# Kernel tuning notes

Measured on AMD Instinct MI355X. Metric: run time of the kernel, lower is better.

The kernel has to match this reference:

```python
import jax, jax.numpy as jnp
import numpy as np

N = 50000      # nodes
E = 800000     # edges (before self loops)
D_IN = 128
HID = 64
HEADS = 8
D_OUT = 10


def setup_inputs() -> dict:
    key = jax.random.key(0)
    ks = jax.random.split(key, 16)
    sc = 0.05
    x = jax.random.normal(ks[0], (N, D_IN), dtype=jnp.float32)
    edge_index = jax.random.randint(ks[1], (2, E), 0, N, dtype=jnp.int64)
    return {
        "x": x,
        "edge_index": edge_index,
        "W1": jax.random.normal(ks[2], (HEADS * HID, D_IN), dtype=jnp.float32) * sc,
        "a1_src": jax.random.normal(ks[3], (HEADS, HID), dtype=jnp.float32) * sc,
        "a1_dst": jax.random.normal(ks[4], (HEADS, HID), dtype=jnp.float32) * sc,
        "b1": jnp.zeros((HEADS * HID,), jnp.float32),
        "W2": jax.random.normal(ks[5], (HID, HEADS * HID), dtype=jnp.float32) * sc,
        "a2_src": jax.random.normal(ks[6], (1, HID), dtype=jnp.float32) * sc,
        "a2_dst": jax.random.normal(ks[7], (1, HID), dtype=jnp.float32) * sc,
        "b2": jnp.zeros((HID,), jnp.float32),
        "W3": jax.random.normal(ks[8], (HID, HID), dtype=jnp.float32) * sc,
        "a3_src": jax.random.normal(ks[9], (1, HID), dtype=jnp.float32) * sc,
        "a3_dst": jax.random.normal(ks[10], (1, HID), dtype=jnp.float32) * sc,
        "b3": jnp.zeros((HID,), jnp.float32),
        "Wc": jax.random.normal(ks[11], (D_OUT, HID), dtype=jnp.float32) * sc,
        "bc": jnp.zeros((D_OUT,), jnp.float32),
    }


def gat_conv(x, src, dst, W, a_src, a_dst, b, concat):
    """PyG GATConv (eval mode, add_self_loops already applied to src/dst)."""
    heads, out_ch = a_src.shape
    n = x.shape[0]
    h = (x @ W.T).reshape(n, heads, out_ch)          # [N, H, C]
    a_s = jnp.einsum('nhc,hc->nh', h, a_src)          # [N, H]
    a_d = jnp.einsum('nhc,hc->nh', h, a_dst)          # [N, H]
    e = jax.nn.leaky_relu(a_s[src] + a_d[dst], 0.2)   # [Etot, H]
    # segment softmax over incoming edges of each destination node
    m = jax.ops.segment_max(e, dst, num_segments=n)
    ex = jnp.exp(e - m[dst])
    s = jax.ops.segment_sum(ex, dst, num_segments=n)
    alpha = ex / (s[dst] + 1e-16)                     # [Etot, H]
    out = jax.ops.segment_sum(h[src] * alpha[:, :, None], dst, num_segments=n)
    if concat:
        out = out.reshape(n, heads * out_ch)
    else:
        out = out.mean(axis=1)
    return out + b


def reference(x, edge_index, W1, a1_src, a1_dst, b1, W2, a2_src, a2_dst, b2,
              W3, a3_src, a3_dst, b3, Wc, bc):
    loops = jnp.arange(N, dtype=edge_index.dtype)
    src = jnp.concatenate([edge_index[0], loops])
    dst = jnp.concatenate([edge_index[1], loops])
    h = jax.nn.elu(gat_conv(x, src, dst, W1, a1_src, a1_dst, b1, True))
    h = jax.nn.elu(gat_conv(h, src, dst, W2, a2_src, a2_dst, b2, False))
    h = jax.nn.elu(gat_conv(h, src, dst, W3, a3_src, a3_dst, b3, False))
    return h @ Wc.T + bc
```

## Files before the change

kernel.cpp:

```cpp
#include <hip/hip_runtime.h>
#include <math.h>

#define N_NODES 50000
#define N_EDGES 800000
#define ETOT    (N_EDGES + N_NODES)
#define COL_CAP (ETOT + 3 * N_NODES + 64)

typedef short bf16x8 __attribute__((ext_vector_type(8)));
typedef float f32x4  __attribute__((ext_vector_type(4)));
typedef float f32x2  __attribute__((ext_vector_type(2)));

__device__ __forceinline__ float b2f(unsigned int u16) {
    return __uint_as_float(u16 << 16);
}
__device__ __forceinline__ unsigned short f2b(float f) {
    unsigned int u = __float_as_uint(f);
    u += 0x7fffu + ((u >> 16) & 1u);
    return (unsigned short)(u >> 16);
}

__global__ __launch_bounds__(256) void k_prep(const float* __restrict__ x,
                                              const float* __restrict__ w1,
                                              const float* __restrict__ w2,
                                              const float* __restrict__ w3,
                                              const float* __restrict__ a1s,
                                              const float* __restrict__ a1d,
                                              unsigned short* __restrict__ xb,
                                              unsigned short* __restrict__ o1,
                                              unsigned short* __restrict__ o2,
                                              unsigned short* __restrict__ o3,
                                              float* __restrict__ U,
                                              int* __restrict__ deg,
                                              int* __restrict__ flag) {
    int i = blockIdx.x * 256 + threadIdx.x;
    if (i < N_NODES) deg[i] = 0;
    if (i == 0) *flag = 0;
    if (blockIdx.x < 8) {
        int h = blockIdx.x;
        int which = threadIdx.x >> 7, k = threadIdx.x & 127;
        const float* av = which ? a1d : a1s;
        float acc = 0.f;
        for (int c = 0; c < 64; ++c)
            acc += av[h * 64 + c] * w1[(size_t)(h * 64 + c) * 128 + k];
        U[(which * 8 + h) * 128 + k] = acc;
    }
    if (i < 512 * 128 / 4) {
        float4 v = ((const float4*)w1)[i];
        ushort2* o = (ushort2*)(o1 + i * 4);
        o[0] = make_ushort2(f2b(v.x), f2b(v.y));
        o[1] = make_ushort2(f2b(v.z), f2b(v.w));
    }
    if (i < 64 * 512 / 4) {
        float4 v = ((const float4*)w2)[i];
        ushort2* o = (ushort2*)(o2 + i * 4);
        o[0] = make_ushort2(f2b(v.x), f2b(v.y));
        o[1] = make_ushort2(f2b(v.z), f2b(v.w));
    }
    if (i < 64 * 64 / 4) {
        float4 v = ((const float4*)w3)[i];
        ushort2* o = (ushort2*)(o3 + i * 4);
        o[0] = make_ushort2(f2b(v.x), f2b(v.y));
        o[1] = make_ushort2(f2b(v.z), f2b(v.w));
    }
    if (i < N_NODES * 128 / 8) {
        const float4* xp = (const float4*)x + (size_t)i * 2;
        float4 v0 = xp[0], v1 = xp[1];
        unsigned int u0 = (unsigned int)f2b(v0.x) | ((unsigned int)f2b(v0.y) << 16);
        unsigned int u1 = (unsigned int)f2b(v0.z) | ((unsigned int)f2b(v0.w) << 16);
        unsigned int u2 = (unsigned int)f2b(v1.x) | ((unsigned int)f2b(v1.y) << 16);
        unsigned int u3 = (unsigned int)f2b(v1.z) | ((unsigned int)f2b(v1.w) << 16);
        *(uint4*)(xb + (size_t)i * 8) = make_uint4(u0, u1, u2, u3);
    }
}

__global__ __launch_bounds__(256) void k_attn(const unsigned short* __restrict__ xb,
                                              const float* __restrict__ U,
                                              float* __restrict__ asrc,
                                              float* __restrict__ adst) {
    __shared__ float sU[16 * 132];
    __shared__ unsigned short sX[16 * 136];
    int t = threadIdx.x;
    for (int i = t; i < 2048; i += 256) sU[(i >> 7) * 132 + (i & 127)] = U[i];
    int n0 = blockIdx.x * 16;
    {
        int r = t >> 4, c = (t & 15) * 8;
        *(uint4*)&sX[r * 136 + c] = *(const uint4*)(xb + (size_t)(n0 + r) * 128 + c);
    }
    __syncthreads();
    int nl = t >> 4, o = t & 15;
    const unsigned short* xr = sX + nl * 136;
    const float* ur = sU + o * 132;
    float acc = 0.f;
#pragma unroll 8
    for (int k2 = 0; k2 < 128; ++k2) acc += b2f(xr[k2]) * ur[k2];
    int n = n0 + nl;
    if (o < 8) asrc[n * 8 + o] = acc;
    else       adst[n * 8 + (o - 8)] = acc;
}

__global__ void k_detect(const int* __restrict__ idx, int* __restrict__ flag) {
    int i = blockIdx.x * blockDim.x + threadIdx.x;
    int v = idx[2 * i + 1];
    unsigned long long any = __ballot(v != 0);
    if ((threadIdx.x & 63) == 0 && any) atomicOr(flag, 1);
}

__device__ __forceinline__ int edge_src(const int* idx, int e, int is32) {
    return is32 ? idx[e] : idx[2 * e];
}
__device__ __forceinline__ int edge_dst(const int* idx, int e, int is32) {
    return is32 ? idx[N_EDGES + e] : idx[2 * (N_EDGES + e)];
}

__global__ void k_degree(const int* __restrict__ idx, const int* __restrict__ flag,
                         int* __restrict__ deg) {
    int e = blockIdx.x * blockDim.x + threadIdx.x;
    if (e >= ETOT) return;
    int is32 = *flag;
    int d = (e < N_EDGES) ? edge_dst(idx, e, is32) : (e - N_EDGES);
    atomicAdd(&deg[d], 1);
}

__global__ __launch_bounds__(256) void k_scan1(const int* __restrict__ deg,
                                               int* __restrict__ rowptr,
                                               int* __restrict__ bsum) {
    __shared__ int sd[256];
    int t = threadIdx.x;
    int i = blockIdx.x * 256 + t;
    int v = (i < N_NODES) ? ((deg[i] + 3) & ~3) : 0;
    sd[t] = v;
    __syncthreads();
#pragma unroll
    for (int off = 1; off < 256; off <<= 1) {
        int a = (t >= off) ? sd[t - off] : 0;
        __syncthreads();
        sd[t] += a;
        __syncthreads();
    }
    if (i < N_NODES) rowptr[i] = sd[t] - v;
    if (t == 255) bsum[blockIdx.x] = sd[255];
}

__global__ __launch_bounds__(256) void k_scan2(int* __restrict__ bsum,
                                               int* __restrict__ boff,
                                               int* __restrict__ rowptr,
                                               int nb) {
    __shared__ int sd[256];
    int t = threadIdx.x;
    int v = (t < nb) ? bsum[t] : 0;
    sd[t] = v;
    __syncthreads();
#pragma unroll
    for (int off = 1; off < 256; off <<= 1) {
        int a = (t >= off) ? sd[t - off] : 0;
        __syncthreads();
        sd[t] += a;
        __syncthreads();
    }
    boff[t] = sd[t] - v;
    if (t == 255) rowptr[N_NODES] = sd[255];
}

__global__ __launch_bounds__(256) void k_scan3(int* __restrict__ rowptr,
                                               const int* __restrict__ boff,
                                               const int* __restrict__ deg,
                                               int* __restrict__ cursor,
                                               int* __restrict__ col) {
    int i = blockIdx.x * 256 + threadIdx.x;
    if (i == 0) {
        int tot = rowptr[N_NODES];
        for (int q = 0; q < 48; ++q) col[tot + q] = 0;
    }
    if (i >= N_NODES) return;
    int r = rowptr[i] + boff[blockIdx.x];
    rowptr[i] = r;
    cursor[i] = r;
    int d = deg[i];
    int pd = (d + 3) & ~3;
    for (int p = r + d; p < r + pd; ++p) col[p] = 0;
}

__global__ void k_scatter(const int* __restrict__ idx, const int* __restrict__ flag,
                          int* __restrict__ cursor, int* __restrict__ col) {
    int e = blockIdx.x * blockDim.x + threadIdx.x;
    if (e >= ETOT) return;
    int is32 = *flag;
    int s, d;
    if (e < N_EDGES) { s = edge_src(idx, e, is32); d = edge_dst(idx, e, is32); }
    else             { s = d = e - N_EDGES; }
    int pos = atomicAdd(&cursor[d], 1);
    col[pos] = s;
}

__device__ __forceinline__ void aggx_slot(int idx, int rem, float tt, unsigned int xx,
                                          float adn, float& ssum, f32x2* acc) {
    float e = tt + adn;
    e = fmaxf(e, 0.2f * e);
    float ex = __expf(e);
    ex = (idx < rem) ? ex : 0.f;
    ssum += ex;
    f32x2 fxy;
    fxy.x = __uint_as_float(xx << 16);
    fxy.y = __uint_as_float(xx & 0xffff0000u);
    int exi = __float_as_int(ex);
#pragma unroll
    for (int hh = 0; hh < 8; ++hh) {
        unsigned int wu = (unsigned int)__builtin_amdgcn_readlane(exi, hh << 3);
        unsigned long long wp = (unsigned long long)wu | ((unsigned long long)wu << 32);
        asm("v_pk_fma_f32 %0, %1, %2, %0" : "+v"(acc[hh]) : "v"(fxy), "s"(wp));
    }
}

__global__ __launch_bounds__(256) void k_aggx(const unsigned short* __restrict__ xb,
                                              const float* __restrict__ asrc,
                                              const float* __restrict__ adst,
                                              const int* __restrict__ rowptr,
                                              const int* __restrict__ degv,
                                              const int* __restrict__ col,
                                              unsigned short* __restrict__ aggX) {
    int n = blockIdx.x * 4 + (threadIdx.x >> 6);
    if (n >= N_NODES) return;
    int l = threadIdx.x & 63;
    int j = l >> 3;
    unsigned lx2 = (unsigned)(l << 1);
    int start = rowptr[n];
    int end   = start + degv[n];
    float adn = adst[((unsigned)n << 3) + (unsigned)j];

    float ssum = 0.f;
    f32x2 acc[8];
#pragma unroll
    for (int hh = 0; hh < 8; ++hh) acc[hh] = (f32x2){0.f, 0.f};

    float tA0, tA1, tA2, tA3, tB0, tB1, tB2, tB3;
    unsigned int xA0, xA1, xA2, xA3, xB0, xB1, xB2, xB3;
    int4 cA, cB;

#define GATHX(c, T0, T1, T2, T3, X0, X1, X2, X3)                              \
    T0 = asrc[(((unsigned)(c).x) << 3) + (unsigned)j];                        \
    T1 = asrc[(((unsigned)(c).y) << 3) + (unsigned)j];                        \
    T2 = asrc[(((unsigned)(c).z) << 3) + (unsigned)j];                        \
    T3 = asrc[(((unsigned)(c).w) << 3) + (unsigned)j];                        \
    X0 = *(const unsigned int*)(xb + (((unsigned)(c).x) << 7) + lx2);         \
    X1 = *(const unsigned int*)(xb + (((unsigned)(c).y) << 7) + lx2);         \
    X2 = *(const unsigned int*)(xb + (((unsigned)(c).z) << 7) + lx2);         \
    X3 = *(const unsigned int*)(xb + (((unsigned)(c).w) << 7) + lx2);

    int k = start;
    cA = *(const int4*)(col + k);
    cB = *(const int4*)(col + k + 4);
    GATHX(cA, tA0, tA1, tA2, tA3, xA0, xA1, xA2, xA3);
    for (;;) {
        bool hasB = (k + 4 < end);
        if (hasB) {
            GATHX(cB, tB0, tB1, tB2, tB3, xB0, xB1, xB2, xB3);
            cA = *(const int4*)(col + k + 8);
        }
        {
            int rem = end - k;
            aggx_slot(0, rem, tA0, xA0, adn, ssum, acc);
            aggx_slot(1, rem, tA1, xA1, adn, ssum, acc);
            aggx_slot(2, rem, tA2, xA2, adn, ssum, acc);
            aggx_slot(3, rem, tA3, xA3, adn, ssum, acc);
        }
        k += 4;
        if (!hasB) break;
        bool hasA = (k + 4 < end);
        if (hasA) {
            GATHX(cA, tA0, tA1, tA2, tA3, xA0, xA1, xA2, xA3);
            cB = *(const int4*)(col + k + 8);
        }
        {
            int rem = end - k;
            aggx_slot(0, rem, tB0, xB0, adn, ssum, acc);
            aggx_slot(1, rem, tB1, xB1, adn, ssum, acc);
            aggx_slot(2, rem, tB2, xB2, adn, ssum, acc);
            aggx_slot(3, rem, tB3, xB3, adn, ssum, acc);
        }
        k += 4;
        if (!hasA) break;
    }
#undef GATHX

    size_t base = (size_t)n * 1024 + lx2;
#pragma unroll
    for (int hh = 0; hh < 8; ++hh) {
        float sh = __int_as_float(__builtin_amdgcn_readlane(__float_as_int(ssum), hh << 3));
        float iv = 1.f / (sh + 1e-16f);
        unsigned int lo = f2b(acc[hh].x * iv);
        unsigned int hi = f2b(acc[hh].y * iv);
        *(unsigned int*)(aggX + base + hh * 128) = lo | (hi << 16);
    }
}

__global__ __launch_bounds__(512, 4) void k_gemm12(const unsigned short* __restrict__ aggX,
                                                   const unsigned short* __restrict__ W1b,
                                                   const float* __restrict__ b1,
                                                   const unsigned short* __restrict__ W2b,
                                                   const float* __restrict__ a2s,
                                                   const float* __restrict__ a2d,
                                                   unsigned short* __restrict__ h2,
                                                   float* __restrict__ asb,
                                                   float* __restrict__ adb) {
    __shared__ unsigned short X2s[64 * 520];
    __shared__ float red_s[8][16];
    __shared__ float red_d[8][16];
    int t = threadIdx.x;
    int w = t >> 6, l = t & 63;
    int quad = l >> 4, lm = l & 15;
    int m0 = blockIdx.x * 64;

    {
        int h = w;
        f32x4 acc1[4][4];
#pragma unroll
        for (int rt = 0; rt < 4; ++rt)
#pragma unroll
            for (int ct = 0; ct < 4; ++ct) acc1[rt][ct] = (f32x4){0.f, 0.f, 0.f, 0.f};

#pragma unroll
        for (int k0 = 0; k0 < 4; ++k0) {
            bf16x8 af[4];
#pragma unroll
            for (int rt = 0; rt < 4; ++rt) {
                int m = m0 + rt * 16 + lm;
                uint4 au = make_uint4(0, 0, 0, 0);
                if (m < N_NODES)
                    au = *(const uint4*)(aggX + (size_t)m * 1024 + h * 128 + k0 * 32 + quad * 8);
                af[rt] = *(bf16x8*)&au;
            }
#pragma unroll
            for (int ct = 0; ct < 4; ++ct) {
                uint4 bu = *(const uint4*)(W1b + (size_t)(h * 64 + ct * 16 + lm) * 128 + k0 * 32 + quad * 8);
                bf16x8 bf_ = *(bf16x8*)&bu;
#pragma unroll
                for (int rt = 0; rt < 4; ++rt)
                    acc1[rt][ct] = __builtin_amdgcn_mfma_f32_16x16x32_bf16(af[rt], bf_, acc1[rt][ct], 0, 0, 0);
            }
        }
#pragma unroll
        for (int ct = 0; ct < 4; ++ct) {
            float bcol = b1[h * 64 + ct * 16 + lm];
#pragma unroll
            for (int rt = 0; rt < 4; ++rt)
#pragma unroll
                for (int g = 0; g < 4; ++g) {
                    float v = acc1[rt][ct][g] + bcol;
                    v = (v > 0.f) ? v : expm1f(v);
                    X2s[(rt * 16 + quad * 4 + g) * 520 + h * 64 + ct * 16 + lm] = f2b(v);
                }
        }
    }
    __syncthreads();

    int rt2 = w >> 1;
    int ct0 = (w & 1) * 2, ct1 = ct0 + 1;
    f32x4 acc2a = (f32x4){0.f, 0.f, 0.f, 0.f};
    f32x4 acc2b = (f32x4){0.f, 0.f, 0.f, 0.f};
#pragma unroll 4
    for (int k0 = 0; k0 < 512; k0 += 32) {
        bf16x8 af = *(const bf16x8*)&X2s[(rt2 * 16 + lm) * 520 + k0 + quad * 8];
        uint4 b0 = *(const uint4*)(W2b + (size_t)(ct0 * 16 + lm) * 512 + k0 + quad * 8);
        uint4 b1u = *(const uint4*)(W2b + (size_t)(ct1 * 16 + lm) * 512 + k0 + quad * 8);
        acc2a = __builtin_amdgcn_mfma_f32_16x16x32_bf16(af, *(bf16x8*)&b0, acc2a, 0, 0, 0);
        acc2b = __builtin_amdgcn_mfma_f32_16x16x32_bf16(af, *(bf16x8*)&b1u, acc2b, 0, 0, 0);
    }

#pragma unroll
    for (int g = 0; g < 4; ++g) {
        int m = m0 + rt2 * 16 + quad * 4 + g;
        if (m < N_NODES) {
            h2[(size_t)m * 64 + ct0 * 16 + lm] = f2b(acc2a[g]);
            h2[(size_t)m * 64 + ct1 * 16 + lm] = f2b(acc2b[g]);
        }
    }

    {
        float as0 = a2s[ct0 * 16 + lm], ad0 = a2d[ct0 * 16 + lm];
        float as1 = a2s[ct1 * 16 + lm], ad1 = a2d[ct1 * 16 + lm];
#pragma unroll
        for (int g = 0; g < 4; ++g) {
            float vs = acc2a[g] * as0 + acc2b[g] * as1;
            float vd = acc2a[g] * ad0 + acc2b[g] * ad1;
#pragma unroll
            for (int off = 1; off < 16; off <<= 1) {
                vs += __shfl_xor(vs, off);
                vd += __shfl_xor(vd, off);
            }
            if (lm == 0) {
                red_s[w][quad * 4 + g] = vs;
                red_d[w][quad * 4 + g] = vd;
            }
        }
    }
    __syncthreads();
    if (t < 64) {
        int rt = t >> 4, rr = t & 15;
        float vs = red_s[2 * rt][rr] + red_s[2 * rt + 1][rr];
        float vd = red_d[2 * rt][rr] + red_d[2 * rt + 1][rr];
        int m = m0 + t;
        if (m < N_NODES) {
            asb[m] = vs;
            adb[m] = vd;
        }
    }
}

__global__ __launch_bounds__(256) void k_gemm(const unsigned short* __restrict__ Ab,
                                              const unsigned short* __restrict__ W,
                                              unsigned short* __restrict__ C,
                                              const float* __restrict__ a_src,
                                              const float* __restrict__ a_dst,
                                              float* __restrict__ asb,
                                              float* __restrict__ adb,
                                              int M, int K, int Nout) {
    __shared__ unsigned short As[64 * 40];
    __shared__ unsigned short Bs[64 * 40];
    __shared__ float red_s[4][64];
    __shared__ float red_d[4][64];
    int t = threadIdx.x;
    int w = t >> 6, l = t & 63;
    int quad = l >> 4, lm = l & 15;
    int m0 = blockIdx.y * 64, n0 = blockIdx.x * 64;
    int lr = t >> 2;
    int lc = (t & 3) * 8;

    f32x4 acc[4];
#pragma unroll
    for (int r = 0; r < 4; ++r) acc[r] = (f32x4){0.f, 0.f, 0.f, 0.f};

    for (int k0 = 0; k0 < K; k0 += 32) {
        int m = m0 + lr;
        uint4 av = make_uint4(0, 0, 0, 0);
        if (m < M) av = *(const uint4*)(Ab + (size_t)m * K + k0 + lc);
        *(uint4*)&As[lr * 40 + lc] = av;
        uint4 bv = *(const uint4*)(W + (size_t)(n0 + lr) * K + k0 + lc);
        *(uint4*)&Bs[lr * 40 + lc] = bv;
        __syncthreads();

        bf16x8 bfrag = *(const bf16x8*)&Bs[(w * 16 + lm) * 40 + quad * 8];
#pragma unroll
        for (int r = 0; r < 4; ++r) {
            bf16x8 afrag = *(const bf16x8*)&As[(r * 16 + lm) * 40 + quad * 8];
            acc[r] = __builtin_amdgcn_mfma_f32_16x16x32_bf16(afrag, bfrag, acc[r], 0, 0, 0);
        }
        __syncthreads();
    }

#pragma unroll
    for (int r = 0; r < 4; ++r)
#pragma unroll
        for (int g = 0; g < 4; ++g) {
            int m = m0 + r * 16 + quad * 4 + g;
            if (m < M) C[(size_t)m * Nout + n0 + w * 16 + lm] = f2b(acc[r][g]);
        }

    float as = a_src[w * 16 + lm];
    float ad = a_dst[w * 16 + lm];
#pragma unroll
    for (int r = 0; r < 4; ++r) {
#pragma unroll
        for (int g = 0; g < 4; ++g) {
            float vs = acc[r][g] * as;
            float vd = acc[r][g] * ad;
#pragma unroll
            for (int off = 1; off < 16; off <<= 1) {
                vs += __shfl_xor(vs, off);
                vd += __shfl_xor(vd, off);
            }
            if (lm == 0) {
                red_s[w][r * 16 + quad * 4 + g] = vs;
                red_d[w][r * 16 + quad * 4 + g] = vd;
            }
        }
    }
    __syncthreads();
    if (t < 64) {
        float vs = red_s[0][t] + red_s[1][t] + red_s[2][t] + red_s[3][t];
        float vd = red_d[0][t] + red_d[1][t] + red_d[2][t] + red_d[3][t];
        int m = m0 + t;
        if (m < M) {
            asb[m] = vs;
            adb[m] = vd;
        }
    }
}

__global__ __launch_bounds__(256) void k_agg1(const unsigned short* __restrict__ h,
                                              const float* __restrict__ asrc,
                                              const float* __restrict__ adst,
                                              const int* __restrict__ rowptr,
                                              const int* __restrict__ degv,
                                              const int* __restrict__ col,
                                              const float* __restrict__ bias,
                                              unsigned short* __restrict__ out) {
    int n = blockIdx.x * 4 + (threadIdx.x >> 6);
    if (n >= N_NODES) return;
    int l = threadIdx.x & 63;
    int start = rowptr[n];
    int end   = start + degv[n];
    float adn = adst[n];

    float ssum = 0.f, o = 0.f;
    float tA0, tA1, tA2, tA3, tB0, tB1, tB2, tB3;
    unsigned short qA0, qA1, qA2, qA3, qB0, qB1, qB2, qB3;
    int4 cA, cB;

#define GATH1(c, T0, T1, T2, T3, Q0, Q1, Q2, Q3)                              \
    T0 = asrc[(unsigned)(c).x];                                               \
    T1 = asrc[(unsigned)(c).y];                                               \
    T2 = asrc[(unsigned)(c).z];                                               \
    T3 = asrc[(unsigned)(c).w];                                               \
    Q0 = h[(((unsigned)(c).x) << 6) + (unsigned)l];                           \
    Q1 = h[(((unsigned)(c).y) << 6) + (unsigned)l];                           \
    Q2 = h[(((unsigned)(c).z) << 6) + (unsigned)l];                           \
    Q3 = h[(((unsigned)(c).w) << 6) + (unsigned)l];

#define ASLOT1(IDX, TT, QQ, rem)                                              \
    {                                                                         \
        float e = TT + adn;                                                   \
        e = fmaxf(e, 0.2f * e);                                               \
        float ex = __expf(e);                                                 \
        ex = ((IDX) < (rem)) ? ex : 0.f;                                      \
        ssum += ex;                                                           \
        o += ex * b2f(QQ);                                                    \
    }

    int k = start;
    cA = *(const int4*)(col + k);
    cB = *(const int4*)(col + k + 4);
    GATH1(cA, tA0, tA1, tA2, tA3, qA0, qA1, qA2, qA3);
    for (;;) {
        bool hasB = (k + 4 < end);
        if (hasB) {
            GATH1(cB, tB0, tB1, tB2, tB3, qB0, qB1, qB2, qB3);
            cA = *(const int4*)(col + k + 8);
        }
        {
            int rem = end - k;
            ASLOT1(0, tA0, qA0, rem);
            ASLOT1(1, tA1, qA1, rem);
            ASLOT1(2, tA2, qA2, rem);
            ASLOT1(3, tA3, qA3, rem);
        }
        k += 4;
        if (!hasB) break;
        bool hasA = (k + 4 < end);
        if (hasA) {
            GATH1(cA, tA0, tA1, tA2, tA3, qA0, qA1, qA2, qA3);
            cB = *(const int4*)(col + k + 8);
        }
        {
            int rem = end - k;
            ASLOT1(0, tB0, qB0, rem);
            ASLOT1(1, tB1, qB1, rem);
            ASLOT1(2, tB2, qB2, rem);
            ASLOT1(3, tB3, qB3, rem);
        }
        k += 4;
        if (!hasA) break;
    }
#undef GATH1
#undef ASLOT1

    float v = o / (ssum + 1e-16f) + bias[l];
    v = (v > 0.f) ? v : expm1f(v);
    out[(size_t)n * 64 + l] = f2b(v);
}

__global__ __launch_bounds__(256) void k_classifier(const unsigned short* __restrict__ h,
                                                    const float* __restrict__ Wc,
                                                    const float* __restrict__ bc,
                                                    float* __restrict__ out) {
    __shared__ float sW[640];
    for (int i = threadIdx.x; i < 640; i += blockDim.x) sW[i] = Wc[i];
    __syncthreads();
    int idx = blockIdx.x * blockDim.x + threadIdx.x;
    if (idx >= N_NODES * 10) return;
    int n = idx / 10, d = idx - n * 10;
    const unsigned short* hr = h + (size_t)n * 64;
    const float* wr = sW + d * 64;
    float acc = 0.f;
#pragma unroll
    for (int c = 0; c < 64; ++c) acc += b2f(hr[c]) * wr[c];
    out[idx] = acc + bc[d];
}

extern "C" void kernel_launch(void* const* d_in, const int* in_sizes, int n_in,
                              void* d_out, int out_size, void* d_ws, size_t ws_size,
                              hipStream_t stream) {
    const float* x    = (const float*)d_in[0];
    const int*   eidx = (const int*)  d_in[1];
    const float* W1   = (const float*)d_in[2];
    const float* a1s  = (const float*)d_in[3];
    const float* a1d  = (const float*)d_in[4];
    const float* b1   = (const float*)d_in[5];
    const float* W2   = (const float*)d_in[6];
    const float* a2s  = (const float*)d_in[7];
    const float* a2d  = (const float*)d_in[8];
    const float* b2   = (const float*)d_in[9];
    const float* W3   = (const float*)d_in[10];
    const float* a3s  = (const float*)d_in[11];
    const float* a3d  = (const float*)d_in[12];
    const float* b3   = (const float*)d_in[13];
    const float* Wc   = (const float*)d_in[14];
    const float* bc   = (const float*)d_in[15];
    float* out = (float*)d_out;

    float* asbuf = (float*)d_ws;
    float* adbuf = asbuf + (size_t)N_NODES * 8;
    unsigned short* aggX = (unsigned short*)(adbuf + (size_t)N_NODES * 8);
    unsigned short* h2  = aggX + (size_t)N_NODES * 1024;
    unsigned short* x3  = h2  + (size_t)N_NODES * 64;
    unsigned short* h3  = x3  + (size_t)N_NODES * 64;
    unsigned short* x4  = h3  + (size_t)N_NODES * 64;
    unsigned short* xb  = x4  + (size_t)N_NODES * 64;
    unsigned short* W1b = xb  + (size_t)N_NODES * 128;
    unsigned short* W2b = W1b + 512 * 128;
    unsigned short* W3b = W2b + 64 * 512;
    float* U    = (float*)(W3b + 64 * 64);
    int* ibase  = (int*)(U + 16 * 128);
    int* deg    = ibase;
    int* flag   = deg + N_NODES;
    int* rowptr = flag + 1;
    int* cursor = rowptr + N_NODES + 1;
    int* bsum   = cursor + N_NODES;
    int* boff   = bsum + 256;
    int* col    = boff + 256;

    dim3 blk(256);
    const int SCAN_BLOCKS = (N_NODES + 255) / 256;
    const int PREP_BLOCKS = (N_NODES * 128 / 8 + 255) / 256;

    k_prep<<<PREP_BLOCKS, blk, 0, stream>>>(x, W1, W2, W3, a1s, a1d,
                                            xb, W1b, W2b, W3b, U, deg, flag);
    k_attn<<<N_NODES / 16, blk, 0, stream>>>(xb, U, asbuf, adbuf);

    k_detect<<<32, blk, 0, stream>>>(eidx, flag);
    k_degree<<<(ETOT + 255) / 256, blk, 0, stream>>>(eidx, flag, deg);
    k_scan1<<<SCAN_BLOCKS, blk, 0, stream>>>(deg, rowptr, bsum);
    k_scan2<<<1, blk, 0, stream>>>(bsum, boff, rowptr, SCAN_BLOCKS);
    k_scan3<<<SCAN_BLOCKS, blk, 0, stream>>>(rowptr, boff, deg, cursor, col);
    k_scatter<<<(ETOT + 255) / 256, blk, 0, stream>>>(eidx, flag, cursor, col);

    int mblocks   = (N_NODES + 63) / 64;
    int nblocks   = N_NODES / 4;

    k_aggx<<<nblocks, blk, 0, stream>>>(xb, asbuf, adbuf, rowptr, deg, col, aggX);

    k_gemm12<<<mblocks, dim3(512), 0, stream>>>(aggX, W1b, b1, W2b, a2s, a2d,
                                                h2, asbuf, adbuf);

    k_agg1<<<nblocks, blk, 0, stream>>>(h2, asbuf, adbuf, rowptr, deg, col, b2, x3);

    k_gemm<<<dim3(1, mblocks), blk, 0, stream>>>(x3, W3b, h3,
                                                 a3s, a3d, asbuf, adbuf,
                                                 N_NODES, 64, 64);
    k_agg1<<<nblocks, blk, 0, stream>>>(h3, asbuf, adbuf, rowptr, deg, col, b3, x4);

    k_classifier<<<(N_NODES * 10 + 255) / 256, blk, 0, stream>>>(x4, Wc, bc, out);
}
```

Before: 435.3 us.

## Remap aggx lanes so each lane owns one head and 16 channels

The layer-1 aggregation kernel changes its lane-to-work mapping. Before, each lane loaded 4 bytes of a source row and broadcast each head's weight with readlane. Now each lane handles one head and loads 32 bytes of that row in two 16-byte vector loads. This removes the cross-lane readlane broadcasts and per-head normalisation shuffles, and stores the output as two 16-byte writes. The trade-off is much higher register use for the in-flight gather buffers (16 uint4 values), which may lower occupancy, and a redundant exp per head is computed in every lane.

```diff
diff --git a/kernel.cpp b/kernel.cpp
--- a/kernel.cpp
+++ b/kernel.cpp
@@ -192,23 +192,32 @@
     col[pos] = s;
 }
 
-__device__ __forceinline__ void aggx_slot(int idx, int rem, float tt, unsigned int xx,
+__device__ __forceinline__ void aggx_slot(int idx, int rem, float tt,
+                                          uint4 ua, uint4 ub,
                                           float adn, float& ssum, f32x2* acc) {
     float e = tt + adn;
     e = fmaxf(e, 0.2f * e);
     float ex = __expf(e);
     ex = (idx < rem) ? ex : 0.f;
     ssum += ex;
-    f32x2 fxy;
-    fxy.x = __uint_as_float(xx << 16);
-    fxy.y = __uint_as_float(xx & 0xffff0000u);
-    int exi = __float_as_int(ex);
-#pragma unroll
-    for (int hh = 0; hh < 8; ++hh) {
-        unsigned int wu = (unsigned int)__builtin_amdgcn_readlane(exi, hh << 3);
-        unsigned long long wp = (unsigned long long)wu | ((unsigned long long)wu << 32);
-        asm("v_pk_fma_f32 %0, %1, %2, %0" : "+v"(acc[hh]) : "v"(fxy), "s"(wp));
-    }
+    f32x2 ex2 = {ex, ex};
+    f32x2 f;
+    f.x = __uint_as_float(ua.x << 16); f.y = __uint_as_float(ua.x & 0xffff0000u);
+    asm("v_pk_fma_f32 %0, %1, %2, %0" : "+v"(acc[0]) : "v"(f), "v"(ex2));
+    f.x = __uint_as_float(ua.y << 16); f.y = __uint_as_float(ua.y & 0xffff0000u);
+    asm("v_pk_fma_f32 %0, %1, %2, %0" : "+v"(acc[1]) : "v"(f), "v"(ex2));
+    f.x = __uint_as_float(ua.z << 16); f.y = __uint_as_float(ua.z & 0xffff0000u);
+    asm("v_pk_fma_f32 %0, %1, %2, %0" : "+v"(acc[2]) : "v"(f), "v"(ex2));
+    f.x = __uint_as_float(ua.w << 16); f.y = __uint_as_float(ua.w & 0xffff0000u);
+    asm("v_pk_fma_f32 %0, %1, %2, %0" : "+v"(acc[3]) : "v"(f), "v"(ex2));
+    f.x = __uint_as_float(ub.x << 16); f.y = __uint_as_float(ub.x & 0xffff0000u);
+    asm("v_pk_fma_f32 %0, %1, %2, %0" : "+v"(acc[4]) : "v"(f), "v"(ex2));
+    f.x = __uint_as_float(ub.y << 16); f.y = __uint_as_float(ub.y & 0xffff0000u);
+    asm("v_pk_fma_f32 %0, %1, %2, %0" : "+v"(acc[5]) : "v"(f), "v"(ex2));
+    f.x = __uint_as_float(ub.z << 16); f.y = __uint_as_float(ub.z & 0xffff0000u);
+    asm("v_pk_fma_f32 %0, %1, %2, %0" : "+v"(acc[6]) : "v"(f), "v"(ex2));
+    f.x = __uint_as_float(ub.w << 16); f.y = __uint_as_float(ub.w & 0xffff0000u);
+    asm("v_pk_fma_f32 %0, %1, %2, %0" : "+v"(acc[7]) : "v"(f), "v"(ex2));
 }
 
 __global__ __launch_bounds__(256) void k_aggx(const unsigned short* __restrict__ xb,
@@ -222,7 +231,7 @@
     if (n >= N_NODES) return;
     int l = threadIdx.x & 63;
     int j = l >> 3;
-    unsigned lx2 = (unsigned)(l << 1);
+    unsigned cs = (unsigned)((l & 7) << 4);
     int start = rowptr[n];
     int end   = start + degv[n];
     float adn = adst[((unsigned)n << 3) + (unsigned)j];
@@ -230,67 +239,75 @@
     float ssum = 0.f;
     f32x2 acc[8];
 #pragma unroll
-    for (int hh = 0; hh < 8; ++hh) acc[hh] = (f32x2){0.f, 0.f};
+    for (int p = 0; p < 8; ++p) acc[p] = (f32x2){0.f, 0.f};
 
     float tA0, tA1, tA2, tA3, tB0, tB1, tB2, tB3;
-    unsigned int xA0, xA1, xA2, xA3, xB0, xB1, xB2, xB3;
+    uint4 xA0a, xA0b, xA1a, xA1b, xA2a, xA2b, xA3a, xA3b;
+    uint4 xB0a, xB0b, xB1a, xB1b, xB2a, xB2b, xB3a, xB3b;
     int4 cA, cB;
 
-#define GATHX(c, T0, T1, T2, T3, X0, X1, X2, X3)                              \
+#define GATHX(c, T0, T1, T2, T3, A0, B0, A1, B1, A2, B2, A3, B3)              \
     T0 = asrc[(((unsigned)(c).x) << 3) + (unsigned)j];                        \
     T1 = asrc[(((unsigned)(c).y) << 3) + (unsigned)j];                        \
     T2 = asrc[(((unsigned)(c).z) << 3) + (unsigned)j];                        \
     T3 = asrc[(((unsigned)(c).w) << 3) + (unsigned)j];                        \
-    X0 = *(const unsigned int*)(xb + (((unsigned)(c).x) << 7) + lx2);         \
-    X1 = *(const unsigned int*)(xb + (((unsigned)(c).y) << 7) + lx2);         \
-    X2 = *(const unsigned int*)(xb + (((unsigned)(c).z) << 7) + lx2);         \
-    X3 = *(const unsigned int*)(xb + (((unsigned)(c).w) << 7) + lx2);
+    A0 = *(const uint4*)(xb + (((unsigned)(c).x) << 7) + cs);                 \
+    B0 = *(const uint4*)(xb + (((unsigned)(c).x) << 7) + cs + 8);             \
+    A1 = *(const uint4*)(xb + (((unsigned)(c).y) << 7) + cs);                 \
+    B1 = *(const uint4*)(xb + (((unsigned)(c).y) << 7) + cs + 8);             \
+    A2 = *(const uint4*)(xb + (((unsigned)(c).z) << 7) + cs);                 \
+    B2 = *(const uint4*)(xb + (((unsigned)(c).z) << 7) + cs + 8);             \
+    A3 = *(const uint4*)(xb + (((unsigned)(c).w) << 7) + cs);                 \
+    B3 = *(const uint4*)(xb + (((unsigned)(c).w) << 7) + cs + 8);
 
     int k = start;
     cA = *(const int4*)(col + k);
     cB = *(const int4*)(col + k + 4);
-    GATHX(cA, tA0, tA1, tA2, tA3, xA0, xA1, xA2, xA3);
+    GATHX(cA, tA0, tA1, tA2, tA3, xA0a, xA0b, xA1a, xA1b, xA2a, xA2b, xA3a, xA3b);
     for (;;) {
         bool hasB = (k + 4 < end);
         if (hasB) {
-            GATHX(cB, tB0, tB1, tB2, tB3, xB0, xB1, xB2, xB3);
+            GATHX(cB, tB0, tB1, tB2, tB3, xB0a, xB0b, xB1a, xB1b, xB2a, xB2b, xB3a, xB3b);
             cA = *(const int4*)(col + k + 8);
         }
         {
             int rem = end - k;
-            aggx_slot(0, rem, tA0, xA0, adn, ssum, acc);
-            aggx_slot(1, rem, tA1, xA1, adn, ssum, acc);
-            aggx_slot(2, rem, tA2, xA2, adn, ssum, acc);
-            aggx_slot(3, rem, tA3, xA3, adn, ssum, acc);
+            aggx_slot(0, rem, tA0, xA0a, xA0b, adn, ssum, acc);
+            aggx_slot(1, rem, tA1, xA1a, xA1b, adn, ssum, acc);
+            aggx_slot(2, rem, tA2, xA2a, xA2b, adn, ssum, acc);
+            aggx_slot(3, rem, tA3, xA3a, xA3b, adn, ssum, acc);
         }
         k += 4;
         if (!hasB) break;
         bool hasA = (k + 4 < end);
         if (hasA) {
-            GATHX(cA, tA0, tA1, tA2, tA3, xA0, xA1, xA2, xA3);
+            GATHX(cA, tA0, tA1, tA2, tA3, xA0a, xA0b, xA1a, xA1b, xA2a, xA2b, xA3a, xA3b);
             cB = *(const int4*)(col + k + 8);
         }
         {
             int rem = end - k;
-            aggx_slot(0, rem, tB0, xB0, adn, ssum, acc);
-            aggx_slot(1, rem, tB1, xB1, adn, ssum, acc);
-            aggx_slot(2, rem, tB2, xB2, adn, ssum, acc);
-            aggx_slot(3, rem, tB3, xB3, adn, ssum, acc);
+            aggx_slot(0, rem, tB0, xB0a, xB0b, adn, ssum, acc);
+            aggx_slot(1, rem, tB1, xB1a, xB1b, adn, ssum, acc);
+            aggx_slot(2, rem, tB2, xB2a, xB2b, adn, ssum, acc);
+            aggx_slot(3, rem, tB3, xB3a, xB3b, adn, ssum, acc);
         }
         k += 4;
         if (!hasA) break;
     }
 #undef GATHX
 
-    size_t base = (size_t)n * 1024 + lx2;
-#pragma unroll
-    for (int hh = 0; hh < 8; ++hh) {
-        float sh = __int_as_float(__builtin_amdgcn_readlane(__float_as_int(ssum), hh << 3));
-        float iv = 1.f / (sh + 1e-16f);
-        unsigned int lo = f2b(acc[hh].x * iv);
-        unsigned int hi = f2b(acc[hh].y * iv);
-        *(unsigned int*)(aggX + base + hh * 128) = lo | (hi << 16);
-    }
+    float iv = 1.f / (ssum + 1e-16f);
+    size_t base = (size_t)n * 1024 + ((unsigned)j << 7) + cs;
+    unsigned int p0 = (unsigned int)f2b(acc[0].x * iv) | ((unsigned int)f2b(acc[0].y * iv) << 16);
+    unsigned int p1 = (unsigned int)f2b(acc[1].x * iv) | ((unsigned int)f2b(acc[1].y * iv) << 16);
+    unsigned int p2 = (unsigned int)f2b(acc[2].x * iv) | ((unsigned int)f2b(acc[2].y * iv) << 16);
+    unsigned int p3 = (unsigned int)f2b(acc[3].x * iv) | ((unsigned int)f2b(acc[3].y * iv) << 16);
+    *(uint4*)(aggX + base) = make_uint4(p0, p1, p2, p3);
+    unsigned int p4 = (unsigned int)f2b(acc[4].x * iv) | ((unsigned int)f2b(acc[4].y * iv) << 16);
+    unsigned int p5 = (unsigned int)f2b(acc[5].x * iv) | ((unsigned int)f2b(acc[5].y * iv) << 16);
+    unsigned int p6 = (unsigned int)f2b(acc[6].x * iv) | ((unsigned int)f2b(acc[6].y * iv) << 16);
+    unsigned int p7 = (unsigned int)f2b(acc[7].x * iv) | ((unsigned int)f2b(acc[7].y * iv) << 16);
+    *(uint4*)(aggX + base + 8) = make_uint4(p4, p5, p6, p7);
 }
 
 __global__ __launch_bounds__(512, 4) void k_gemm12(const unsigned short* __restrict__ aggX,
```

Measured after the change: 456.7 us. 1.05x slower.
